# Kernel tuning notes

Hardware: AMD Instinct MI355X
Metric: run time of the kernel (lower is better)

The kernel has to match this reference:

```python
import jax, jax.numpy as jnp
import numpy as np

HID = 2048
NH = 16
HD = HID // NH
FF = 8192
SEQ = 2048
B = 1
EPS = 1e-05
ROPE_BASE = 10000.0


def _layernorm(x, w, b):
    mu = jnp.mean(x, axis=-1, keepdims=True)
    var = jnp.mean(jnp.square(x - mu), axis=-1, keepdims=True)
    return (x - mu) * jax.lax.rsqrt(var + EPS) * w + b


def _rope(x, offset):
    # x: [B, S, H, D]; rotate-half LLaMA-style rotary embedding
    S, D = x.shape[1], x.shape[3]
    inv_freq = 1.0 / (ROPE_BASE ** (jnp.arange(0, D, 2, dtype=jnp.float32) / D))  # [D/2]
    pos = jnp.arange(S, dtype=jnp.float32) + offset
    ang = pos[:, None] * inv_freq[None, :]                     # [S, D/2]
    cos = jnp.cos(ang)[None, :, None, :]                       # [1,S,1,D/2]
    sin = jnp.sin(ang)[None, :, None, :]
    x1, x2 = x[..., : D // 2], x[..., D // 2 :]
    return jnp.concatenate([x1 * cos - x2 * sin, x2 * cos + x1 * sin], axis=-1)


def setup_inputs() -> dict:
    key = jax.random.key(0)
    ks = jax.random.split(key, 16)
    sd = 0.02
    inp = {
        "hidden_states": jax.random.normal(ks[0], (B, SEQ, HID), dtype=jnp.float32),
        # additive causal mask as fed to multi_head_attention_forward
        "attention_mask": jnp.where(
            jnp.tril(jnp.ones((SEQ, SEQ), dtype=bool)), 0.0, -1e9
        ).astype(jnp.float32),
        "ln1_w": jnp.ones((HID,), jnp.float32),
        "ln1_b": jnp.zeros((HID,), jnp.float32),
        "ln2_w": jnp.ones((HID,), jnp.float32),
        "ln2_b": jnp.zeros((HID,), jnp.float32),
        "wq": jax.random.normal(ks[1], (HID, HID), jnp.float32) * sd,
        "bq": jnp.zeros((HID,), jnp.float32),
        "wk": jax.random.normal(ks[2], (HID, HID), jnp.float32) * sd,
        "bk": jnp.zeros((HID,), jnp.float32),
        "wv": jax.random.normal(ks[3], (HID, HID), jnp.float32) * sd,
        "bv": jnp.zeros((HID,), jnp.float32),
        "wo": jax.random.normal(ks[4], (HID, HID), jnp.float32) * sd,
        "bo": jnp.zeros((HID,), jnp.float32),
        "w_gate": jax.random.normal(ks[5], (FF, HID), jnp.float32) * sd,
        "w_up": jax.random.normal(ks[6], (FF, HID), jnp.float32) * sd,
        "w_down": jax.random.normal(ks[7], (HID, FF), jnp.float32) * sd,
        "total_seq_len": SEQ,
    }
    return inp


def reference(hidden_states, attention_mask, ln1_w, ln1_b, ln2_w, ln2_b,
              wq, bq, wk, bk, wv, bv, wo, bo, w_gate, w_up, w_down,
              total_seq_len):
    Bv, S, _ = hidden_states.shape
    x = _layernorm(hidden_states, ln1_w, ln1_b)
    q = (x @ wq.T + bq).reshape(Bv, S, NH, HD)
    k = (x @ wk.T + bk).reshape(Bv, S, NH, HD)
    v = (x @ wv.T + bv).reshape(Bv, S, NH, HD)
    offset = total_seq_len - S  # 0 for prefill
    q = _rope(q, offset)
    k = _rope(k, offset)
    # cache of max_sequence_length zeros concatenated with k/v then sliced to the
    # last total_seq_len entries == just the current k/v when total_seq_len == S
    scale = 1.0 / np.sqrt(HD)
    scores = jnp.einsum("bshd,bthd->bhst", q, k) * scale + attention_mask[None, None]
    probs = jax.nn.softmax(scores, axis=-1)
    attn = jnp.einsum("bhst,bthd->bshd", probs, v).reshape(Bv, S, HID)
    attn = attn @ wo.T + bo
    h = hidden_states + attn
    y = _layernorm(h, ln2_w, ln2_b)
    ffn = (jax.nn.silu(y @ w_gate.T) * (y @ w_up.T)) @ w_down.T
    return h + ffn
```

## Files before the change

### kernel.cpp

```cpp
#include <hip/hip_runtime.h>

#define HIDN 2048
#define NHEAD 16
#define HDIM 128
#define FFDIM 8192
#define SEQLEN 2048

typedef __attribute__((ext_vector_type(8))) __bf16 bf16x8;
typedef __attribute__((ext_vector_type(4))) float f32x4;
typedef __attribute__((ext_vector_type(4))) unsigned short u16x4;
typedef __attribute__((ext_vector_type(8))) unsigned short u16x8;

__device__ __forceinline__ unsigned short f2bfu(float f) {
    unsigned int u = __float_as_uint(f);
    unsigned int r = u + 0x7fffu + ((u >> 16) & 1u);
    return (unsigned short)(r >> 16);
}
__device__ __forceinline__ float bfu2f(unsigned short u) {
    return __uint_as_float(((unsigned int)u) << 16);
}

__device__ __forceinline__ void gload16(const void* g, void* l) {
    __builtin_amdgcn_global_load_lds(
        (const __attribute__((address_space(1))) unsigned int*)g,
        (__attribute__((address_space(3))) unsigned int*)l,
        16, 0, 0);
}

__global__ __launch_bounds__(256)
void conv_f32_bf16(const float* __restrict__ src, unsigned short* __restrict__ dst) {
    int i = blockIdx.x * 256 + threadIdx.x;
    float4 a = ((const float4*)src)[i * 2];
    float4 b = ((const float4*)src)[i * 2 + 1];
    u16x8 v;
    v[0] = f2bfu(a.x); v[1] = f2bfu(a.y); v[2] = f2bfu(a.z); v[3] = f2bfu(a.w);
    v[4] = f2bfu(b.x); v[5] = f2bfu(b.y); v[6] = f2bfu(b.z); v[7] = f2bfu(b.w);
    *(u16x8*)(dst + (size_t)i * 8) = v;
}

__global__ __launch_bounds__(256)
void conv3_f32_bf16(const float* __restrict__ s0, const float* __restrict__ s1,
                    const float* __restrict__ s2, unsigned short* __restrict__ dst) {
    int i = blockIdx.x * 256 + threadIdx.x;
    int m = i >> 19;
    int li = i & ((1 << 19) - 1);
    const float* s = (m == 0) ? s0 : (m == 1) ? s1 : s2;
    float4 a = ((const float4*)s)[li * 2];
    float4 b = ((const float4*)s)[li * 2 + 1];
    u16x8 v;
    v[0] = f2bfu(a.x); v[1] = f2bfu(a.y); v[2] = f2bfu(a.z); v[3] = f2bfu(a.w);
    v[4] = f2bfu(b.x); v[5] = f2bfu(b.y); v[6] = f2bfu(b.z); v[7] = f2bfu(b.w);
    *(u16x8*)(dst + (size_t)i * 8) = v;
}

__global__ __launch_bounds__(256)
void ln_bf16(const float* __restrict__ x, const float* __restrict__ w,
             const float* __restrict__ b, unsigned short* __restrict__ out) {
    const int row = blockIdx.x;
    const int tid = threadIdx.x;
    const float* xr = x + (size_t)row * HIDN;
    float4 v0 = ((const float4*)xr)[tid];
    float4 v1 = ((const float4*)xr)[tid + 256];
    float s = v0.x + v0.y + v0.z + v0.w + v1.x + v1.y + v1.z + v1.w;
    float q = v0.x*v0.x + v0.y*v0.y + v0.z*v0.z + v0.w*v0.w
            + v1.x*v1.x + v1.y*v1.y + v1.z*v1.z + v1.w*v1.w;
    for (int o = 32; o > 0; o >>= 1) {
        s += __shfl_down(s, o, 64);
        q += __shfl_down(q, o, 64);
    }
    __shared__ float red[8];
    const int wid = tid >> 6;
    if ((tid & 63) == 0) { red[wid] = s; red[4 + wid] = q; }
    __syncthreads();
    float st = red[0] + red[1] + red[2] + red[3];
    float qt = red[4] + red[5] + red[6] + red[7];
    float mu = st * (1.0f / HIDN);
    float var = qt * (1.0f / HIDN) - mu * mu;
    float rs = rsqrtf(var + 1e-5f);
    unsigned short* orow = out + (size_t)row * HIDN;
    int i0 = tid * 4, i1 = (tid + 256) * 4;
    orow[i0 + 0] = f2bfu((v0.x - mu) * rs * w[i0 + 0] + b[i0 + 0]);
    orow[i0 + 1] = f2bfu((v0.y - mu) * rs * w[i0 + 1] + b[i0 + 1]);
    orow[i0 + 2] = f2bfu((v0.z - mu) * rs * w[i0 + 2] + b[i0 + 2]);
    orow[i0 + 3] = f2bfu((v0.w - mu) * rs * w[i0 + 3] + b[i0 + 3]);
    orow[i1 + 0] = f2bfu((v1.x - mu) * rs * w[i1 + 0] + b[i1 + 0]);
    orow[i1 + 1] = f2bfu((v1.y - mu) * rs * w[i1 + 1] + b[i1 + 1]);
    orow[i1 + 2] = f2bfu((v1.z - mu) * rs * w[i1 + 2] + b[i1 + 2]);
    orow[i1 + 3] = f2bfu((v1.w - mu) * rs * w[i1 + 3] + b[i1 + 3]);
}

__global__ __launch_bounds__(256)
void rope_kernel(unsigned short* __restrict__ qk, const int* __restrict__ tsl) {
    int id = blockIdx.x * 256 + threadIdx.x;
    int p  = id & 63;
    int hh = (id >> 6) & 31;
    int s  = id >> 11;
    int off = tsl[0] - SEQLEN;
    float inv = exp2f((float)p * -0.20762050593f);
    float ang = (float)(s + off) * inv;
    float c, sn;
    __sincosf(ang, &sn, &c);
    size_t base = (size_t)s * 4096 + hh * 128 + p;
    float x1 = bfu2f(qk[base]);
    float x2 = bfu2f(qk[base + 64]);
    qk[base]      = f2bfu(x1 * c - x2 * sn);
    qk[base + 64] = f2bfu(x2 * c + x1 * sn);
}

#define BAR __builtin_amdgcn_s_barrier()
#define VM4 asm volatile("s_waitcnt vmcnt(4)" ::: "memory")
#define VM0 asm volatile("s_waitcnt vmcnt(0)" ::: "memory")
#define LGK4 do { asm volatile("s_waitcnt lgkmcnt(4)" ::: "memory"); \
                  __builtin_amdgcn_sched_barrier(0); } while (0)
#define LGK0 do { asm volatile("s_waitcnt lgkmcnt(0)" ::: "memory"); \
                  __builtin_amdgcn_sched_barrier(0); } while (0)

#define STAGE_A(tile, h) { const int k0_ = k_start + (tile) * 64;                      \
  _Pragma("unroll") for (int i_ = 0; i_ < 2; ++i_) {                                   \
    int d_ = (h) * 16384 + i_ * 8192 + tid * 16;                                       \
    int r_ = d_ >> 7;                                                                  \
    int cb_ = (d_ & 127) ^ ((r_ & 7) << 4);                                            \
    gload16((const char*)Ab + ((size_t)(brow + r_) * lda + k0_) * 2 + cb_,             \
            smem + ((tile) & 1) * 65536 + (h) * 16384 + i_ * 8192 + w * 1024); } }

#define STAGE_B(tile, h) { const int k0_ = k_start + (tile) * 64;                      \
  _Pragma("unroll") for (int i_ = 0; i_ < 2; ++i_) {                                   \
    int d_ = (h) * 16384 + i_ * 8192 + tid * 16;                                       \
    int r_ = d_ >> 7;                                                                  \
    int cb_ = (d_ & 127) ^ ((r_ & 7) << 4);                                            \
    gload16((const char*)Bb + ((size_t)(bcol + r_) * ldb + k0_) * 2 + cb_,             \
            smem + ((tile) & 1) * 65536 + 32768 + (h) * 16384 + i_ * 8192 + w * 1024); } }

#define LDB(BO)                                                                        \
  _Pragma("unroll") for (int n_ = 0; n_ < 4; ++n_)                                     \
  _Pragma("unroll") for (int kk_ = 0; kk_ < 2; ++kk_)                                  \
    bF[n_][kk_] = *(const bf16x8*)(smem + (BO) + bbase + n_ * 2048 + colb[kk_]);

#define LDA_SET(BO, MP, SET)                                                           \
  _Pragma("unroll") for (int dm_ = 0; dm_ < 2; ++dm_)                                  \
  _Pragma("unroll") for (int kk_ = 0; kk_ < 2; ++kk_)                                  \
    SET[dm_][kk_] = *(const bf16x8*)(smem + (BO) + abase + ((MP) * 2 + dm_) * 2048 + colb[kk_]);

#define MM_SET(SET, MP)                                                                \
  __builtin_amdgcn_s_setprio(1);                                                       \
  _Pragma("unroll") for (int dm_ = 0; dm_ < 2; ++dm_)                                  \
  _Pragma("unroll") for (int n_ = 0; n_ < 4; ++n_)                                     \
  _Pragma("unroll") for (int kk_ = 0; kk_ < 2; ++kk_)                                  \
    acc[(MP) * 2 + dm_][n_] = __builtin_amdgcn_mfma_f32_16x16x32_bf16(                 \
        SET[dm_][kk_], bF[n_][kk_], acc[(MP) * 2 + dm_][n_], 0, 0, 0);                 \
  __builtin_amdgcn_s_setprio(0);

template<int EPI>
__global__ __launch_bounds__(512, 1)
void gemm256(const unsigned short* __restrict__ Ab, int lda,
             const unsigned short* __restrict__ Bb, int ldb,
             int k_len, int nbx, int ldc,
             const float* __restrict__ bias0, const float* __restrict__ bias1,
             const float* __restrict__ bias2,
             unsigned short* __restrict__ outB, unsigned short* __restrict__ outV) {
    extern __shared__ char smem[];
    const int tid = threadIdx.x;
    const int w = tid >> 6, lane = tid & 63;
    const int lr = lane & 15, lg = lane >> 4;
    const int wrow = (w >> 2) * 128;
    const int wc = w & 3;

    const int cpx = nbx >> 3;
    const int xcd = blockIdx.x & 7;
    const int loc = blockIdx.x >> 3;
    const int bx = xcd * cpx + loc % cpx;
    const int by = loc / cpx;
    const int brow = by * 256, bcol = bx * 256;
    const int k_start = blockIdx.y * k_len;

    const int xorv = (lr & 7) << 4;
    int colb[2];
    colb[0] = (lg * 16) ^ xorv;
    colb[1] = (64 + lg * 16) ^ xorv;
    const int abase = (wrow + lr) * 128;
    const int bbase = 32768 + (wc * 64 + lr) * 128;

    f32x4 acc[8][4];
#pragma unroll
    for (int m = 0; m < 8; ++m)
#pragma unroll
        for (int n = 0; n < 4; ++n) acc[m][n] = (f32x4){0.f, 0.f, 0.f, 0.f};

    bf16x8 bF[4][2], aFa[2][2], aFb[2][2];

    const int NT = k_len >> 6;
    const int NIT = NT >> 1;

    STAGE_A(0, 0); STAGE_A(0, 1); STAGE_B(0, 0); STAGE_B(0, 1);
    STAGE_B(1, 0); STAGE_B(1, 1);
    VM4; BAR;
    LDB(0); LDA_SET(0, 0, aFa);

    for (int it = 0; it < NIT; ++it) {
        const int T = 2 * it;
        const bool s2 = (T + 2) < NT, s3 = (T + 3) < NT;
        STAGE_A(T + 1, 0); LDA_SET(0, 1, aFb); LGK4; MM_SET(aFa, 0);
        STAGE_A(T + 1, 1); LDA_SET(0, 2, aFa); LGK4; MM_SET(aFb, 1);
        BAR;
        if (s2) STAGE_B(T + 2, 0);
        LDA_SET(0, 3, aFb); LGK4; MM_SET(aFa, 2);
        if (s2) STAGE_B(T + 2, 1);
        LGK0; MM_SET(aFb, 3);
        if (s2) { VM4; } else { VM0; }
        BAR;
        LDB(65536); LDA_SET(65536, 0, aFa);
        if (s2) STAGE_A(T + 2, 0);
        LDA_SET(65536, 1, aFb); LGK4; MM_SET(aFa, 0);
        if (s2) STAGE_A(T + 2, 1);
        LDA_SET(65536, 2, aFa); LGK4; MM_SET(aFb, 1);
        BAR;
        if (s3) STAGE_B(T + 3, 0);
        LDA_SET(65536, 3, aFb); LGK4; MM_SET(aFa, 2);
        if (s3) STAGE_B(T + 3, 1);
        LGK0; MM_SET(aFb, 3);
        if (s3) { VM4; } else { VM0; }
        BAR;
        LDB(0); LDA_SET(0, 0, aFa);
    }

    char* sw = smem + w * 16384;
    const bool vblk = (EPI == 0) && (bcol >= 4096);

    if (!vblk) {
#pragma unroll
        for (int n = 0; n < 4; ++n) {
            const int col = bcol + wc * 64 + n * 16 + lr;
            float bv = 0.f;
            if (EPI == 0) bv = (col < 2048) ? bias0[col] : bias1[col - 2048];
#pragma unroll
            for (int m = 0; m < 8; ++m)
#pragma unroll
                for (int j = 0; j < 4; ++j) {
                    const int r = m * 16 + lg * 4 + j;
                    const int cb = ((n * 16 + lr) * 2) ^ ((r & 7) << 4);
                    *(unsigned short*)(sw + r * 128 + cb) = f2bfu(acc[m][n][j] + bv);
                }
        }
        const int rl = lane >> 3, cl = lane & 7;
#pragma unroll
        for (int it2 = 0; it2 < 16; ++it2) {
            const int r = it2 * 8 + rl;
            const int cb = (cl * 16) ^ ((r & 7) << 4);
            u16x8 val = *(const u16x8*)(sw + r * 128 + cb);
            const int gr = brow + wrow + r;
            const int gcol = bcol + wc * 64 + cl * 8;
            if (EPI == 0) {
                *(u16x8*)(outB + (size_t)gr * 4096 + gcol) = val;
            } else if (EPI == 1) {
                *(u16x8*)(outB + (size_t)gr * ldc + gcol) = val;
            } else if (EPI == 3) {
                unsigned short* gp = outB + (size_t)gr * ldc + gcol;
                u16x8 gv = *(const u16x8*)gp;
                u16x8 ov;
#pragma unroll
                for (int e = 0; e < 8; ++e) {
                    float g = bfu2f(gv[e]);
                    float uu = bfu2f(val[e]);
                    ov[e] = f2bfu(g / (1.0f + __expf(-g)) * uu);
                }
                *(u16x8*)gp = ov;
            } else {
                *(u16x8*)(outB + (size_t)blockIdx.y * 4194304 + (size_t)gr * ldc + gcol) = val;
            }
        }
    } else {
#pragma unroll
        for (int n = 0; n < 4; ++n) {
            const int c = n * 16 + lr;
            const float bv = bias2[bcol - 4096 + wc * 64 + c];
            const int cx = (c & 7) << 4;
#pragma unroll
            for (int m = 0; m < 8; ++m) {
                const int r0 = m * 16 + lg * 4;
                u16x4 pk;
#pragma unroll
                for (int j = 0; j < 4; ++j) pk[j] = f2bfu(acc[m][n][j] + bv);
                *(u16x4*)(sw + c * 256 + ((r0 * 2) ^ cx)) = pk;
            }
        }
        const int cg = lane >> 4, rl2 = lane & 15;
#pragma unroll
        for (int it2 = 0; it2 < 16; ++it2) {
            const int c = it2 * 4 + cg;
            const int rb = (rl2 * 16) ^ ((c & 7) << 4);
            u16x8 val = *(const u16x8*)(sw + c * 256 + rb);
            const int d = bcol - 4096 + wc * 64 + c;
            *(u16x8*)(outV + (size_t)d * SEQLEN + brow + wrow + rl2 * 8) = val;
        }
    }
}

__global__ __launch_bounds__(256)
void reduce4_add(const unsigned short* __restrict__ part, float* __restrict__ out) {
    int i = blockIdx.x * 256 + threadIdx.x;
    float4 o = ((const float4*)out)[i];
#pragma unroll
    for (int sk = 0; sk < 4; ++sk) {
        u16x4 p = ((const u16x4*)(part + (size_t)sk * 4194304))[i];
        o.x += bfu2f(p[0]); o.y += bfu2f(p[1]); o.z += bfu2f(p[2]); o.w += bfu2f(p[3]);
    }
    ((float4*)out)[i] = o;
}

__global__ __launch_bounds__(256)
void reduce4_wo(const unsigned short* __restrict__ part, const float* __restrict__ h,
                const float* __restrict__ bias, float* __restrict__ out) {
    int i = blockIdx.x * 256 + threadIdx.x;
    float4 o = ((const float4*)h)[i];
    int col = (i & 511) * 4;
    o.x += bias[col]; o.y += bias[col + 1]; o.z += bias[col + 2]; o.w += bias[col + 3];
#pragma unroll
    for (int sk = 0; sk < 4; ++sk) {
        u16x4 p = ((const u16x4*)(part + (size_t)sk * 4194304))[i];
        o.x += bfu2f(p[0]); o.y += bfu2f(p[1]); o.z += bfu2f(p[2]); o.w += bfu2f(p[3]);
    }
    ((float4*)out)[i] = o;
}

#define PST 72
__global__ __launch_bounds__(256)
void attn_kernel(const unsigned short* __restrict__ QK, const unsigned short* __restrict__ VT,
                 unsigned short* __restrict__ O) {
    __shared__ __align__(16) unsigned short Ks[2][64 * 128];
    __shared__ __align__(16) unsigned short Vs[2][128 * 64];
    __shared__ __align__(16) unsigned short Ps[4][16 * PST];
    const int tid = threadIdx.x;
    const int lane = tid & 63;
    const int w = tid >> 6;
    const int lr = lane & 15, lg = lane >> 4;

    const int id = blockIdx.x;
    const int pair = id & 7;
    const int j0 = id >> 3;
    const int h = pair * 2 + (j0 & 1);
    const int qb = 31 - (j0 >> 1);
    const int q0 = qb * 64;
    const int qw = q0 + w * 16;

    const unsigned short* Qb = QK + (size_t)qw * 4096 + h * 128;
    const unsigned short* Kb = QK + 2048 + h * 128;
    const unsigned short* Vb = VT + (size_t)(h * 128) * SEQLEN;

    bf16x8 qa[4];
#pragma unroll
    for (int c = 0; c < 4; ++c)
        qa[c] = *(const bf16x8*)(Qb + (size_t)lr * 4096 + c * 32 + lg * 8);

    int krow[4], kcb[4], vrow[4], vcb[4];
#pragma unroll
    for (int ch = 0; ch < 4; ++ch) {
        int d = ch * 4096 + w * 1024 + lane * 16;
        krow[ch] = d >> 8;
        kcb[ch]  = (d & 255) ^ ((krow[ch] & 7) << 4);
        vrow[ch] = d >> 7;
        vcb[ch]  = (d & 127) ^ ((vrow[ch] & 7) << 4);
    }

    f32x4 acc[8];
#pragma unroll
    for (int dt = 0; dt < 8; ++dt) acc[dt] = (f32x4){0.f, 0.f, 0.f, 0.f};
    float mrow[4] = {-INFINITY, -INFINITY, -INFINITY, -INFINITY};
    float lrow[4] = {0.f, 0.f, 0.f, 0.f};

    const float sc = 0.08838834764831845f;
    const int ntile = qb + 1;

#pragma unroll
    for (int ch = 0; ch < 4; ++ch) {
        gload16(Kb + (size_t)krow[ch] * 4096 + (kcb[ch] >> 1),
                (char*)&Ks[0][0] + ch * 4096 + w * 1024);
        gload16(Vb + (size_t)vrow[ch] * SEQLEN + (vcb[ch] >> 1),
                (char*)&Vs[0][0] + ch * 4096 + w * 1024);
    }
    __syncthreads();

    for (int tt = 0; tt < ntile; ++tt) {
        const int cur = tt & 1;
        const int t0 = tt * 64;
        if (tt + 1 < ntile) {
            const int t1 = t0 + 64;
#pragma unroll
            for (int ch = 0; ch < 4; ++ch) {
                gload16(Kb + (size_t)(t1 + krow[ch]) * 4096 + (kcb[ch] >> 1),
                        (char*)&Ks[cur ^ 1][0] + ch * 4096 + w * 1024);
                gload16(Vb + (size_t)vrow[ch] * SEQLEN + t1 + (vcb[ch] >> 1),
                        (char*)&Vs[cur ^ 1][0] + ch * 4096 + w * 1024);
            }
        }
        f32x4 s[4];
#pragma unroll
        for (int th = 0; th < 4; ++th) s[th] = (f32x4){0.f, 0.f, 0.f, 0.f};
        __builtin_amdgcn_s_setprio(1);
#pragma unroll
        for (int th = 0; th < 4; ++th) {
            const int row = th * 16 + lr;
#pragma unroll
            for (int c = 0; c < 4; ++c) {
                bf16x8 kb = *(const bf16x8*)((char*)&Ks[cur][0] + row * 256 +
                                             ((c * 64 + lg * 16) ^ ((lr & 7) << 4)));
                s[th] = __builtin_amdgcn_mfma_f32_16x16x32_bf16(qa[c], kb, s[th], 0, 0, 0);
            }
        }
        __builtin_amdgcn_s_setprio(0);
#pragma unroll
        for (int th = 0; th < 4; ++th) {
            int tg = t0 + th * 16 + lr;
#pragma unroll
            for (int jj = 0; jj < 4; ++jj) {
                int qg = qw + lg * 4 + jj;
                s[th][jj] = s[th][jj] * sc + (tg <= qg ? 0.f : -1e9f);
            }
        }
        float mt[4];
#pragma unroll
        for (int jj = 0; jj < 4; ++jj)
            mt[jj] = fmaxf(fmaxf(s[0][jj], s[1][jj]), fmaxf(s[2][jj], s[3][jj]));
#pragma unroll
        for (int o = 8; o > 0; o >>= 1)
#pragma unroll
            for (int jj = 0; jj < 4; ++jj) mt[jj] = fmaxf(mt[jj], __shfl_xor(mt[jj], o, 16));
        bool need = false;
#pragma unroll
        for (int jj = 0; jj < 4; ++jj) need = need || (mt[jj] > mrow[jj] + 4.0f);
        if (__any(need)) {
#pragma unroll
            for (int jj = 0; jj < 4; ++jj) {
                float mn = fmaxf(mrow[jj], mt[jj]);
                float a = __expf(mrow[jj] - mn);
                mrow[jj] = mn;
                lrow[jj] *= a;
#pragma unroll
                for (int dt = 0; dt < 8; ++dt) acc[dt][jj] *= a;
            }
        }
        float ps[4] = {0.f, 0.f, 0.f, 0.f};
#pragma unroll
        for (int th = 0; th < 4; ++th)
#pragma unroll
            for (int jj = 0; jj < 4; ++jj) {
                float p = __expf(s[th][jj] - mrow[jj]);
                s[th][jj] = p;
                ps[jj] += p;
            }
#pragma unroll
        for (int o = 8; o > 0; o >>= 1)
#pragma unroll
            for (int jj = 0; jj < 4; ++jj) ps[jj] += __shfl_xor(ps[jj], o, 16);
#pragma unroll
        for (int jj = 0; jj < 4; ++jj) lrow[jj] += ps[jj];
#pragma unroll
        for (int th = 0; th < 4; ++th)
#pragma unroll
            for (int jj = 0; jj < 4; ++jj)
                Ps[w][(lg * 4 + jj) * PST + th * 16 + lr] = f2bfu(s[th][jj]);
        bf16x8 pa[2];
#pragma unroll
        for (int ks = 0; ks < 2; ++ks)
            pa[ks] = *(const bf16x8*)&Ps[w][lr * PST + ks * 32 + lg * 8];
        __builtin_amdgcn_s_setprio(1);
#pragma unroll
        for (int dt = 0; dt < 8; ++dt) {
            const int d = dt * 16 + lr;
#pragma unroll
            for (int ks = 0; ks < 2; ++ks) {
                bf16x8 vb = *(const bf16x8*)((char*)&Vs[cur][0] + d * 128 +
                                             ((ks * 64 + lg * 16) ^ ((lr & 7) << 4)));
                acc[dt] = __builtin_amdgcn_mfma_f32_16x16x32_bf16(pa[ks], vb, acc[dt], 0, 0, 0);
            }
        }
        __builtin_amdgcn_s_setprio(0);
        __syncthreads();
    }
    float invl[4];
#pragma unroll
    for (int jj = 0; jj < 4; ++jj) invl[jj] = 1.0f / lrow[jj];
#pragma unroll
    for (int dt = 0; dt < 8; ++dt)
#pragma unroll
        for (int jj = 0; jj < 4; ++jj)
            O[(size_t)(qw + lg * 4 + jj) * HIDN + h * HDIM + dt * 16 + lr] = f2bfu(acc[dt][jj] * invl[jj]);
}

extern "C" void kernel_launch(void* const* d_in, const int* in_sizes, int n_in,
                              void* d_out, int out_size, void* d_ws, size_t ws_size,
                              hipStream_t stream) {
    const float* hidden = (const float*)d_in[0];
    const float* ln1w = (const float*)d_in[2];
    const float* ln1b = (const float*)d_in[3];
    const float* ln2w = (const float*)d_in[4];
    const float* ln2b = (const float*)d_in[5];
    const float* wq = (const float*)d_in[6];
    const float* bq = (const float*)d_in[7];
    const float* wk = (const float*)d_in[8];
    const float* bk = (const float*)d_in[9];
    const float* wv = (const float*)d_in[10];
    const float* bv = (const float*)d_in[11];
    const float* wo = (const float*)d_in[12];
    const float* bo = (const float*)d_in[13];
    const float* wg = (const float*)d_in[14];
    const float* wu = (const float*)d_in[15];
    const float* wd = (const float*)d_in[16];
    const int* tsl = (const int*)d_in[17];
    float* out = (float*)d_out;

    char* ws = (char*)d_ws;
    const size_t MB = 1024 * 1024;
    unsigned short* Wbuf = (unsigned short*)(ws);
    unsigned short* qk   = (unsigned short*)(ws + 32 * MB);
    unsigned short* vt   = (unsigned short*)(ws + 48 * MB);
    unsigned short* x_bf = (unsigned short*)(ws + 56 * MB);
    unsigned short* g_bf = (unsigned short*)(ws + 64 * MB);
    unsigned short* part = qk;
    unsigned short* y_bf = vt;

    const int HID2 = HIDN * HIDN;
    const int CONV_HID = HID2 / 8 / 256;
    const int CONV_FF  = FFDIM * HIDN / 8 / 256;
    const size_t LDSZ = 131072;

    conv3_f32_bf16<<<3 * CONV_HID, 256, 0, stream>>>(wq, wk, wv, Wbuf);
    ln_bf16<<<SEQLEN, 256, 0, stream>>>(hidden, ln1w, ln1b, x_bf);
    gemm256<0><<<dim3(192, 1), 512, LDSZ, stream>>>(x_bf, HIDN, Wbuf, HIDN, HIDN, 24, 0,
                                                    bq, bk, bv, qk, vt);
    rope_kernel<<<SEQLEN * 32 * 64 / 256, 256, 0, stream>>>(qk, tsl);
    attn_kernel<<<512, 256, 0, stream>>>(qk, vt, x_bf);

    conv_f32_bf16<<<CONV_HID, 256, 0, stream>>>(wo, Wbuf);
    gemm256<4><<<dim3(64, 4), 512, LDSZ, stream>>>(x_bf, HIDN, Wbuf, HIDN, 512, 8, HIDN,
                                                   nullptr, nullptr, nullptr, g_bf, nullptr);
    reduce4_wo<<<4096, 256, 0, stream>>>(g_bf, hidden, bo, out);

    ln_bf16<<<SEQLEN, 256, 0, stream>>>(out, ln2w, ln2b, y_bf);
    conv_f32_bf16<<<CONV_FF, 256, 0, stream>>>(wg, Wbuf);
    gemm256<1><<<dim3(256, 1), 512, LDSZ, stream>>>(y_bf, HIDN, Wbuf, HIDN, HIDN, 32, FFDIM,
                                                    nullptr, nullptr, nullptr, g_bf, nullptr);
    conv_f32_bf16<<<CONV_FF, 256, 0, stream>>>(wu, Wbuf);
    gemm256<3><<<dim3(256, 1), 512, LDSZ, stream>>>(y_bf, HIDN, Wbuf, HIDN, HIDN, 32, FFDIM,
                                                    nullptr, nullptr, nullptr, g_bf, nullptr);
    conv_f32_bf16<<<CONV_FF, 256, 0, stream>>>(wd, Wbuf);
    gemm256<4><<<dim3(64, 4), 512, LDSZ, stream>>>(g_bf, FFDIM, Wbuf, FFDIM, 2048, 8, HIDN,
                                                   nullptr, nullptr, nullptr, part, nullptr);
    reduce4_add<<<4096, 256, 0, stream>>>(part, out);
}
```

Baseline: 449.6 us.

## Pair causal attention query blocks per workgroup and fuse Wo reduce with LN2

```diff
diff --git a/kernel.cpp b/kernel.cpp
--- a/kernel.cpp
+++ b/kernel.cpp
@@ -87,6 +87,55 @@
     orow[i1 + 1] = f2bfu((v1.y - mu) * rs * w[i1 + 1] + b[i1 + 1]);
     orow[i1 + 2] = f2bfu((v1.z - mu) * rs * w[i1 + 2] + b[i1 + 2]);
     orow[i1 + 3] = f2bfu((v1.w - mu) * rs * w[i1 + 3] + b[i1 + 3]);
+}
+
+__global__ __launch_bounds__(256)
+void wo_ln(const unsigned short* __restrict__ part, const float* __restrict__ h,
+           const float* __restrict__ bo, const float* __restrict__ w,
+           const float* __restrict__ b, float* __restrict__ out,
+           unsigned short* __restrict__ ybf) {
+    const int row = blockIdx.x;
+    const int tid = threadIdx.x;
+    const int c0 = tid * 4, c1 = (tid + 256) * 4;
+    float4 o0 = ((const float4*)(h + (size_t)row * HIDN))[tid];
+    float4 o1 = ((const float4*)(h + (size_t)row * HIDN))[tid + 256];
+    o0.x += bo[c0]; o0.y += bo[c0 + 1]; o0.z += bo[c0 + 2]; o0.w += bo[c0 + 3];
+    o1.x += bo[c1]; o1.y += bo[c1 + 1]; o1.z += bo[c1 + 2]; o1.w += bo[c1 + 3];
+#pragma unroll
+    for (int sk = 0; sk < 4; ++sk) {
+        const unsigned short* pr = part + (size_t)sk * 4194304 + (size_t)row * HIDN;
+        u16x4 p0 = *(const u16x4*)(pr + c0);
+        u16x4 p1 = *(const u16x4*)(pr + c1);
+        o0.x += bfu2f(p0[0]); o0.y += bfu2f(p0[1]); o0.z += bfu2f(p0[2]); o0.w += bfu2f(p0[3]);
+        o1.x += bfu2f(p1[0]); o1.y += bfu2f(p1[1]); o1.z += bfu2f(p1[2]); o1.w += bfu2f(p1[3]);
+    }
+    ((float4*)(out + (size_t)row * HIDN))[tid] = o0;
+    ((float4*)(out + (size_t)row * HIDN))[tid + 256] = o1;
+    float s = o0.x + o0.y + o0.z + o0.w + o1.x + o1.y + o1.z + o1.w;
+    float q = o0.x*o0.x + o0.y*o0.y + o0.z*o0.z + o0.w*o0.w
+            + o1.x*o1.x + o1.y*o1.y + o1.z*o1.z + o1.w*o1.w;
+    for (int o = 32; o > 0; o >>= 1) {
+        s += __shfl_down(s, o, 64);
+        q += __shfl_down(q, o, 64);
+    }
+    __shared__ float red[8];
+    const int wid = tid >> 6;
+    if ((tid & 63) == 0) { red[wid] = s; red[4 + wid] = q; }
+    __syncthreads();
+    float st = red[0] + red[1] + red[2] + red[3];
+    float qt = red[4] + red[5] + red[6] + red[7];
+    float mu = st * (1.0f / HIDN);
+    float var = qt * (1.0f / HIDN) - mu * mu;
+    float rs = rsqrtf(var + 1e-5f);
+    unsigned short* yr = ybf + (size_t)row * HIDN;
+    yr[c0 + 0] = f2bfu((o0.x - mu) * rs * w[c0 + 0] + b[c0 + 0]);
+    yr[c0 + 1] = f2bfu((o0.y - mu) * rs * w[c0 + 1] + b[c0 + 1]);
+    yr[c0 + 2] = f2bfu((o0.z - mu) * rs * w[c0 + 2] + b[c0 + 2]);
+    yr[c0 + 3] = f2bfu((o0.w - mu) * rs * w[c0 + 3] + b[c0 + 3]);
+    yr[c1 + 0] = f2bfu((o1.x - mu) * rs * w[c1 + 0] + b[c1 + 0]);
+    yr[c1 + 1] = f2bfu((o1.y - mu) * rs * w[c1 + 1] + b[c1 + 1]);
+    yr[c1 + 2] = f2bfu((o1.z - mu) * rs * w[c1 + 2] + b[c1 + 2]);
+    yr[c1 + 3] = f2bfu((o1.w - mu) * rs * w[c1 + 3] + b[c1 + 3]);
 }
 
 __global__ __launch_bounds__(256)
@@ -307,21 +356,6 @@
     ((float4*)out)[i] = o;
 }
 
-__global__ __launch_bounds__(256)
-void reduce4_wo(const unsigned short* __restrict__ part, const float* __restrict__ h,
-                const float* __restrict__ bias, float* __restrict__ out) {
-    int i = blockIdx.x * 256 + threadIdx.x;
-    float4 o = ((const float4*)h)[i];
-    int col = (i & 511) * 4;
-    o.x += bias[col]; o.y += bias[col + 1]; o.z += bias[col + 2]; o.w += bias[col + 3];
-#pragma unroll
-    for (int sk = 0; sk < 4; ++sk) {
-        u16x4 p = ((const u16x4*)(part + (size_t)sk * 4194304))[i];
-        o.x += bfu2f(p[0]); o.y += bfu2f(p[1]); o.z += bfu2f(p[2]); o.w += bfu2f(p[3]);
-    }
-    ((float4*)out)[i] = o;
-}
-
 #define PST 72
 __global__ __launch_bounds__(256)
 void attn_kernel(const unsigned short* __restrict__ QK, const unsigned short* __restrict__ VT,
@@ -335,21 +369,11 @@
     const int lr = lane & 15, lg = lane >> 4;
 
     const int id = blockIdx.x;
-    const int pair = id & 7;
-    const int j0 = id >> 3;
-    const int h = pair * 2 + (j0 & 1);
-    const int qb = 31 - (j0 >> 1);
-    const int q0 = qb * 64;
-    const int qw = q0 + w * 16;
-
-    const unsigned short* Qb = QK + (size_t)qw * 4096 + h * 128;
+    const int h = ((id & 7) << 1) | ((id >> 3) & 1);
+    const int p = id >> 4;
+
     const unsigned short* Kb = QK + 2048 + h * 128;
     const unsigned short* Vb = VT + (size_t)(h * 128) * SEQLEN;
-
-    bf16x8 qa[4];
-#pragma unroll
-    for (int c = 0; c < 4; ++c)
-        qa[c] = *(const bf16x8*)(Qb + (size_t)lr * 4096 + c * 32 + lg * 8);
 
     int krow[4], kcb[4], vrow[4], vcb[4];
 #pragma unroll
@@ -361,129 +385,142 @@
         vcb[ch]  = (d & 127) ^ ((vrow[ch] & 7) << 4);
     }
 
-    f32x4 acc[8];
-#pragma unroll
-    for (int dt = 0; dt < 8; ++dt) acc[dt] = (f32x4){0.f, 0.f, 0.f, 0.f};
-    float mrow[4] = {-INFINITY, -INFINITY, -INFINITY, -INFINITY};
-    float lrow[4] = {0.f, 0.f, 0.f, 0.f};
-
     const float sc = 0.08838834764831845f;
-    const int ntile = qb + 1;
-
-#pragma unroll
-    for (int ch = 0; ch < 4; ++ch) {
-        gload16(Kb + (size_t)krow[ch] * 4096 + (kcb[ch] >> 1),
-                (char*)&Ks[0][0] + ch * 4096 + w * 1024);
-        gload16(Vb + (size_t)vrow[ch] * SEQLEN + (vcb[ch] >> 1),
-                (char*)&Vs[0][0] + ch * 4096 + w * 1024);
-    }
-    __syncthreads();
-
-    for (int tt = 0; tt < ntile; ++tt) {
-        const int cur = tt & 1;
-        const int t0 = tt * 64;
-        if (tt + 1 < ntile) {
-            const int t1 = t0 + 64;
-#pragma unroll
-            for (int ch = 0; ch < 4; ++ch) {
-                gload16(Kb + (size_t)(t1 + krow[ch]) * 4096 + (kcb[ch] >> 1),
-                        (char*)&Ks[cur ^ 1][0] + ch * 4096 + w * 1024);
-                gload16(Vb + (size_t)vrow[ch] * SEQLEN + t1 + (vcb[ch] >> 1),
-                        (char*)&Vs[cur ^ 1][0] + ch * 4096 + w * 1024);
-            }
+
+#pragma unroll 1
+    for (int seg = 0; seg < 2; ++seg) {
+        const int qb = seg ? (31 - p) : p;
+        const int qw = qb * 64 + w * 16;
+        const unsigned short* Qb = QK + (size_t)qw * 4096 + h * 128;
+
+        bf16x8 qa[4];
+#pragma unroll
+        for (int c = 0; c < 4; ++c)
+            qa[c] = *(const bf16x8*)(Qb + (size_t)lr * 4096 + c * 32 + lg * 8);
+
+        f32x4 acc[8];
+#pragma unroll
+        for (int dt = 0; dt < 8; ++dt) acc[dt] = (f32x4){0.f, 0.f, 0.f, 0.f};
+        float mrow[4] = {-INFINITY, -INFINITY, -INFINITY, -INFINITY};
+        float lrow[4] = {0.f, 0.f, 0.f, 0.f};
+        const int ntile = qb + 1;
+
+#pragma unroll
+        for (int ch = 0; ch < 4; ++ch) {
+            gload16(Kb + (size_t)krow[ch] * 4096 + (kcb[ch] >> 1),
+                    (char*)&Ks[0][0] + ch * 4096 + w * 1024);
+            gload16(Vb + (size_t)vrow[ch] * SEQLEN + (vcb[ch] >> 1),
+                    (char*)&Vs[0][0] + ch * 4096 + w * 1024);
         }
-        f32x4 s[4];
-#pragma unroll
-        for (int th = 0; th < 4; ++th) s[th] = (f32x4){0.f, 0.f, 0.f, 0.f};
-        __builtin_amdgcn_s_setprio(1);
-#pragma unroll
-        for (int th = 0; th < 4; ++th) {
-            const int row = th * 16 + lr;
-#pragma unroll
-            for (int c = 0; c < 4; ++c) {
-                bf16x8 kb = *(const bf16x8*)((char*)&Ks[cur][0] + row * 256 +
-                                             ((c * 64 + lg * 16) ^ ((lr & 7) << 4)));
-                s[th] = __builtin_amdgcn_mfma_f32_16x16x32_bf16(qa[c], kb, s[th], 0, 0, 0);
-            }
+        __syncthreads();
+
+        for (int tt = 0; tt < ntile; ++tt) {
+            const int cur = tt & 1;
+            const int t0 = tt * 64;
+            if (tt + 1 < ntile) {
+                const int t1 = t0 + 64;
+#pragma unroll
+                for (int ch = 0; ch < 4; ++ch) {
+                    gload16(Kb + (size_t)(t1 + krow[ch]) * 4096 + (kcb[ch] >> 1),
+                            (char*)&Ks[cur ^ 1][0] + ch * 4096 + w * 1024);
+                    gload16(Vb + (size_t)vrow[ch] * SEQLEN + t1 + (vcb[ch] >> 1),
+                            (char*)&Vs[cur ^ 1][0] + ch * 4096 + w * 1024);
+                }
+            }
+            f32x4 s[4];
+#pragma unroll
+            for (int th = 0; th < 4; ++th) s[th] = (f32x4){0.f, 0.f, 0.f, 0.f};
+            __builtin_amdgcn_s_setprio(1);
+#pragma unroll
+            for (int th = 0; th < 4; ++th) {
+                const int row = th * 16 + lr;
+#pragma unroll
+                for (int c = 0; c < 4; ++c) {
+                    bf16x8 kb = *(const bf16x8*)((char*)&Ks[cur][0] + row * 256 +
+                                                 ((c * 64 + lg * 16) ^ ((lr & 7) << 4)));
+                    s[th] = __builtin_amdgcn_mfma_f32_16x16x32_bf16(qa[c], kb, s[th], 0, 0, 0);
+                }
+            }
+            __builtin_amdgcn_s_setprio(0);
+#pragma unroll
+            for (int th = 0; th < 4; ++th) {
+                int tg = t0 + th * 16 + lr;
+#pragma unroll
+                for (int jj = 0; jj < 4; ++jj) {
+                    int qg = qw + lg * 4 + jj;
+                    s[th][jj] = s[th][jj] * sc + (tg <= qg ? 0.f : -1e9f);
+                }
+            }
+            float mt[4];
+#pragma unroll
+            for (int jj = 0; jj < 4; ++jj)
+                mt[jj] = fmaxf(fmaxf(s[0][jj], s[1][jj]), fmaxf(s[2][jj], s[3][jj]));
+#pragma unroll
+            for (int o = 8; o > 0; o >>= 1)
+#pragma unroll
+                for (int jj = 0; jj < 4; ++jj) mt[jj] = fmaxf(mt[jj], __shfl_xor(mt[jj], o, 16));
+            bool need = false;
+#pragma unroll
+            for (int jj = 0; jj < 4; ++jj) need = need || (mt[jj] > mrow[jj] + 4.0f);
+            if (__any(need)) {
+#pragma unroll
+                for (int jj = 0; jj < 4; ++jj) {
+                    float mn = fmaxf(mrow[jj], mt[jj]);
+                    float a = __expf(mrow[jj] - mn);
+                    mrow[jj] = mn;
+                    lrow[jj] *= a;
+#pragma unroll
+                    for (int dt = 0; dt < 8; ++dt) acc[dt][jj] *= a;
+                }
+            }
+            float ps[4] = {0.f, 0.f, 0.f, 0.f};
+#pragma unroll
+            for (int th = 0; th < 4; ++th)
+#pragma unroll
+                for (int jj = 0; jj < 4; ++jj) {
+                    float pp = __expf(s[th][jj] - mrow[jj]);
+                    s[th][jj] = pp;
+                    ps[jj] += pp;
+                }
+#pragma unroll
+            for (int o = 8; o > 0; o >>= 1)
+#pragma unroll
+                for (int jj = 0; jj < 4; ++jj) ps[jj] += __shfl_xor(ps[jj], o, 16);
+#pragma unroll
+            for (int jj = 0; jj < 4; ++jj) lrow[jj] += ps[jj];
+#pragma unroll
+            for (int th = 0; th < 4; ++th)
+#pragma unroll
+                for (int jj = 0; jj < 4; ++jj)
+                    Ps[w][(lg * 4 + jj) * PST + th * 16 + lr] = f2bfu(s[th][jj]);
+            bf16x8 pa[2];
+#pragma unroll
+            for (int ks = 0; ks < 2; ++ks)
+                pa[ks] = *(const bf16x8*)&Ps[w][lr * PST + ks * 32 + lg * 8];
+            __builtin_amdgcn_s_setprio(1);
+#pragma unroll
+            for (int dt = 0; dt < 8; ++dt) {
+                const int d = dt * 16 + lr;
+#pragma unroll
+                for (int ks = 0; ks < 2; ++ks) {
+                    bf16x8 vb = *(const bf16x8*)((char*)&Vs[cur][0] + d * 128 +
+                                                 ((ks * 64 + lg * 16) ^ ((lr & 7) << 4)));
+                    acc[dt] = __builtin_amdgcn_mfma_f32_16x16x32_bf16(pa[ks], vb, acc[dt], 0, 0, 0);
+                }
+            }
+            __builtin_amdgcn_s_setprio(0);
+            __syncthreads();
         }
-        __builtin_amdgcn_s_setprio(0);
-#pragma unroll
-        for (int th = 0; th < 4; ++th) {
-            int tg = t0 + th * 16 + lr;
-#pragma unroll
-            for (int jj = 0; jj < 4; ++jj) {
-                int qg = qw + lg * 4 + jj;
-                s[th][jj] = s[th][jj] * sc + (tg <= qg ? 0.f : -1e9f);
-            }
-        }
-        float mt[4];
-#pragma unroll
-        for (int jj = 0; jj < 4; ++jj)
-            mt[jj] = fmaxf(fmaxf(s[0][jj], s[1][jj]), fmaxf(s[2][jj], s[3][jj]));
-#pragma unroll
-        for (int o = 8; o > 0; o >>= 1)
-#pragma unroll
-            for (int jj = 0; jj < 4; ++jj) mt[jj] = fmaxf(mt[jj], __shfl_xor(mt[jj], o, 16));
-        bool need = false;
-#pragma unroll
-        for (int jj = 0; jj < 4; ++jj) need = need || (mt[jj] > mrow[jj] + 4.0f);
-        if (__any(need)) {
-#pragma unroll
-            for (int jj = 0; jj < 4; ++jj) {
-                float mn = fmaxf(mrow[jj], mt[jj]);
-                float a = __expf(mrow[jj] - mn);
-                mrow[jj] = mn;
-                lrow[jj] *= a;
-#pragma unroll
-                for (int dt = 0; dt < 8; ++dt) acc[dt][jj] *= a;
-            }
-        }
-        float ps[4] = {0.f, 0.f, 0.f, 0.f};
-#pragma unroll
-        for (int th = 0; th < 4; ++th)
-#pragma unroll
-            for (int jj = 0; jj < 4; ++jj) {
-                float p = __expf(s[th][jj] - mrow[jj]);
-                s[th][jj] = p;
-                ps[jj] += p;
-            }
-#pragma unroll
-        for (int o = 8; o > 0; o >>= 1)
-#pragma unroll
-            for (int jj = 0; jj < 4; ++jj) ps[jj] += __shfl_xor(ps[jj], o, 16);
-#pragma unroll
-        for (int jj = 0; jj < 4; ++jj) lrow[jj] += ps[jj];
-#pragma unroll
-        for (int th = 0; th < 4; ++th)
+        float invl[4];
+#pragma unroll
+        for (int jj = 0; jj < 4; ++jj) invl[jj] = 1.0f / lrow[jj];
+#pragma unroll
+        for (int dt = 0; dt < 8; ++dt)
 #pragma unroll
             for (int jj = 0; jj < 4; ++jj)
-                Ps[w][(lg * 4 + jj) * PST + th * 16 + lr] = f2bfu(s[th][jj]);
-        bf16x8 pa[2];
-#pragma unroll
-        for (int ks = 0; ks < 2; ++ks)
-            pa[ks] = *(const bf16x8*)&Ps[w][lr * PST + ks * 32 + lg * 8];
-        __builtin_amdgcn_s_setprio(1);
-#pragma unroll
-        for (int dt = 0; dt < 8; ++dt) {
-            const int d = dt * 16 + lr;
-#pragma unroll
-            for (int ks = 0; ks < 2; ++ks) {
-                bf16x8 vb = *(const bf16x8*)((char*)&Vs[cur][0] + d * 128 +
-                                             ((ks * 64 + lg * 16) ^ ((lr & 7) << 4)));
-                acc[dt] = __builtin_amdgcn_mfma_f32_16x16x32_bf16(pa[ks], vb, acc[dt], 0, 0, 0);
-            }
-        }
-        __builtin_amdgcn_s_setprio(0);
-        __syncthreads();
-    }
-    float invl[4];
-#pragma unroll
-    for (int jj = 0; jj < 4; ++jj) invl[jj] = 1.0f / lrow[jj];
-#pragma unroll
-    for (int dt = 0; dt < 8; ++dt)
-#pragma unroll
-        for (int jj = 0; jj < 4; ++jj)
-            O[(size_t)(qw + lg * 4 + jj) * HIDN + h * HDIM + dt * 16 + lr] = f2bfu(acc[dt][jj] * invl[jj]);
+                O[(size_t)(qw + lg * 4 + jj) * HIDN + h * HDIM + dt * 16 + lr] =
+                    f2bfu(acc[dt][jj] * invl[jj]);
+    }
 }
 
 extern "C" void kernel_launch(void* const* d_in, const int* in_sizes, int n_in,
@@ -528,14 +565,13 @@
     gemm256<0><<<dim3(192, 1), 512, LDSZ, stream>>>(x_bf, HIDN, Wbuf, HIDN, HIDN, 24, 0,
                                                     bq, bk, bv, qk, vt);
     rope_kernel<<<SEQLEN * 32 * 64 / 256, 256, 0, stream>>>(qk, tsl);
-    attn_kernel<<<512, 256, 0, stream>>>(qk, vt, x_bf);
+    attn_kernel<<<256, 256, 0, stream>>>(qk, vt, x_bf);
 
     conv_f32_bf16<<<CONV_HID, 256, 0, stream>>>(wo, Wbuf);
     gemm256<4><<<dim3(64, 4), 512, LDSZ, stream>>>(x_bf, HIDN, Wbuf, HIDN, 512, 8, HIDN,
                                                    nullptr, nullptr, nullptr, g_bf, nullptr);
-    reduce4_wo<<<4096, 256, 0, stream>>>(g_bf, hidden, bo, out);
-
-    ln_bf16<<<SEQLEN, 256, 0, stream>>>(out, ln2w, ln2b, y_bf);
+    wo_ln<<<SEQLEN, 256, 0, stream>>>(g_bf, hidden, bo, ln2w, ln2b, out, y_bf);
+
     conv_f32_bf16<<<CONV_FF, 256, 0, stream>>>(wg, Wbuf);
     gemm256<1><<<dim3(256, 1), 512, LDSZ, stream>>>(y_bf, HIDN, Wbuf, HIDN, HIDN, 32, FFDIM,
                                                     nullptr, nullptr, nullptr, g_bf, nullptr);
```

New measurement: 442.2 us. About the same (-1.7%).
